# Performance work log

Hardware: AMD Instinct MI355X
Metric: run time of the kernel (lower is better)

Reference implementation:

```python
import jax, jax.numpy as jnp
import numpy as np

B, S, H, D = 2, 4096, 16, 128  # batch, seq, heads, head_dim
HID = H * D                    # 2048 hidden size
C = 128                        # chunk size for the chunked recurrent scan
EPS = 1e-6


def setup_inputs() -> dict:
    key = jax.random.key(0)
    ks = jax.random.split(key, 9)
    sc = 0.02  # initializer_range
    w = lambda k: jax.random.normal(k, (HID, HID), jnp.float32) * sc
    return {
        "x": jax.random.normal(ks[0], (B, S, HID), jnp.float32),
        "Wq": w(ks[1]), "bq": jnp.zeros((HID,), jnp.float32),
        "Wk": w(ks[2]), "bk": jnp.zeros((HID,), jnp.float32),
        "Wv": w(ks[3]), "bv": jnp.zeros((HID,), jnp.float32),
        "Wo": w(ks[4]), "bo": jnp.zeros((HID,), jnp.float32),
    }


def reference(x, Wq, bq, Wk, bk, Wv, bv, Wo, bo):
    Bx, Sx, hid = x.shape
    NC = Sx // C  # number of chunks

    q = (x @ Wq + bq).reshape(Bx, Sx, H, D)
    k = (x @ Wk + bk).reshape(Bx, Sx, H, D)
    v = (x @ Wv + bv).reshape(Bx, Sx, H, D)

    # positive feature map for linear attention
    qf = jax.nn.elu(q) + 1.0
    kf = jax.nn.elu(k) + 1.0

    # chunk: [B, NC, C, H, D]
    qf = qf.reshape(Bx, NC, C, H, D)
    kf = kf.reshape(Bx, NC, C, H, D)
    vc = v.reshape(Bx, NC, C, H, D)

    # inter-chunk recurrent state: exclusive cumulative sums of per-chunk KV outer
    kv = jnp.einsum('bnchd,bnche->bnhde', kf, vc)      # per-chunk KV state
    kv_ex = jnp.cumsum(kv, axis=1) - kv                # exclusive prefix state
    ksum = kf.sum(axis=2)                              # [B,NC,H,D]
    ksum_ex = jnp.cumsum(ksum, axis=1) - ksum          # exclusive normalizer state

    inter = jnp.einsum('bnchd,bnhde->bnche', qf, kv_ex)
    z_inter = jnp.einsum('bnchd,bnhd->bnch', qf, ksum_ex)

    # intra-chunk causal attention (masked matmul)
    A = jnp.einsum('bnchd,bnkhd->bnhck', qf, kf)       # [B,NC,H,C,C]
    causal = jnp.tril(jnp.ones((C, C), dtype=bool))
    A = jnp.where(causal[None, None, None], A, 0.0)
    intra = jnp.einsum('bnhck,bnkhe->bnche', A, vc)
    z_intra = jnp.swapaxes(A.sum(-1), 2, 3)            # [B,NC,C,H]

    out = (inter + intra) / (z_inter + z_intra + EPS)[..., None]
    out = out.reshape(Bx, Sx, hid)
    return out @ Wo + bo
```

## Files before the change

kernel.cpp:

```cpp
#include <hip/hip_runtime.h>

typedef unsigned short u16;
typedef unsigned int u32;
typedef unsigned long long u64;
typedef __attribute__((ext_vector_type(8))) short short8;
typedef __attribute__((ext_vector_type(4))) float f32x4;
typedef __attribute__((ext_vector_type(4))) int int4v;

constexpr int Bsz = 2, Ssz = 4096, Hn = 16, Dh = 128, HID = 2048;
constexpr int Cch = 128, NCh = 32;
constexpr float EPSf = 1e-6f;

#define MFMA16 __builtin_amdgcn_mfma_f32_16x16x32_bf16
#define VMCNT0 asm volatile("s_waitcnt vmcnt(0)" ::: "memory")

__device__ __forceinline__ float b2f(u16 u) {
  unsigned int i = ((unsigned int)u) << 16;
  return __builtin_bit_cast(float, i);
}
__device__ __forceinline__ u16 f2b(float f) {
  unsigned int i = __builtin_bit_cast(unsigned int, f);
  i += 0x7fffu + ((i >> 16) & 1u);
  return (u16)(i >> 16);
}

__device__ __forceinline__ void gload_lds16(const u16* g, u16* l) {
  __builtin_amdgcn_global_load_lds(
      (const __attribute__((address_space(1))) u32*)g,
      (__attribute__((address_space(3))) u32*)l, 16, 0, 0);
}

__global__ __launch_bounds__(256) void cvt_bf16(const float* __restrict__ x,
                                                u16* __restrict__ xb)
{
  const size_t n8 = (size_t)Bsz * Ssz * HID / 8;
  for (size_t i = (size_t)blockIdx.x * 256 + threadIdx.x; i < n8;
       i += (size_t)gridDim.x * 256) {
    const f32x4 a = *(const f32x4*)&x[i * 8];
    const f32x4 b = *(const f32x4*)&x[i * 8 + 4];
    u16 tmp[8];
#pragma unroll
    for (int u = 0; u < 4; ++u) { tmp[u] = f2b(a[u]); tmp[u + 4] = f2b(b[u]); }
    *(int4v*)&xb[i * 8] = *(const int4v*)tmp;
  }
}

__global__ __launch_bounds__(256) void transpose4(
    const float* __restrict__ A0, const float* __restrict__ A1,
    const float* __restrict__ A2, const float* __restrict__ A3,
    u16* __restrict__ T0, u16* __restrict__ T1,
    u16* __restrict__ T2, u16* __restrict__ T3)
{
  constexpr int N = HID, LDT = 72;
  const int z = blockIdx.z;
  const float* __restrict__ A = (z == 0) ? A0 : (z == 1) ? A1 : (z == 2) ? A2 : A3;
  u16* __restrict__ T = (z == 0) ? T0 : (z == 1) ? T1 : (z == 2) ? T2 : T3;
  __shared__ u16 lds[64 * LDT];
  const int t = threadIdx.x;
  const int i = t >> 3, j = (t & 7) * 8;
  const int r0 = blockIdx.y * 64, c0 = blockIdx.x * 64;
#pragma unroll
  for (int half = 0; half < 2; ++half) {
    const int r = i + half * 32;
    const f32x4 a = *(const f32x4*)&A[(size_t)(r0 + r) * N + c0 + j];
    const f32x4 b = *(const f32x4*)&A[(size_t)(r0 + r) * N + c0 + j + 4];
    u16 tmp[8];
#pragma unroll
    for (int u = 0; u < 4; ++u) { tmp[u] = f2b(a[u]); tmp[u + 4] = f2b(b[u]); }
    *(int4v*)&lds[r * LDT + j] = *(const int4v*)tmp;
  }
  __syncthreads();
#pragma unroll
  for (int half = 0; half < 2; ++half) {
    const int c = i + half * 32;
    u16 tmp[8];
#pragma unroll
    for (int u = 0; u < 8; ++u) tmp[u] = lds[(j + u) * LDT + c];
    *(int4v*)&T[(size_t)(c0 + c) * N + r0 + j] = *(const int4v*)tmp;
  }
}

template <int OUTF32>
__global__ __launch_bounds__(512) void gemm1b(
    const u16* __restrict__ A,
    const u16* __restrict__ W0T, const u16* __restrict__ W1T, const u16* __restrict__ W2T,
    const float* __restrict__ bb0, const float* __restrict__ bb1, const float* __restrict__ bb2,
    void* __restrict__ o0, void* __restrict__ o1, void* __restrict__ o2,
    int elu_mask)
{
  constexpr int K = HID, N = HID;
  constexpr int NT = K / 64;
  extern __shared__ u16 lds[];

  const int z = blockIdx.z;
  const u16* __restrict__ WT    = (z == 0) ? W0T : (z == 1) ? W1T : W2T;
  const float* __restrict__ bias = (z == 0) ? bb0 : (z == 1) ? bb1 : bb2;
  void* __restrict__ outv = (z == 0) ? o0 : (z == 1) ? o1 : o2;
  const bool elu = (elu_mask >> z) & 1;

  const int lid = blockIdx.x + 8 * blockIdx.y;
  const int wlid = (lid & 7) * 32 + (lid >> 3);
  const int n0 = (wlid >> 5) * 256;
  const int m0 = (wlid & 31) * 256;

  const int t = threadIdx.x, lane = t & 63, w = t >> 6;
  const int wm = w >> 2, wn = w & 3;
  const int l15 = lane & 15, lg = lane >> 4;
  const int sl2 = (l15 >> 1) & 3;

  const int strow = lane >> 2;
  const int stslot = (lane & 3) ^ ((lane >> 3) & 3);
  const u16* gA = A  + (size_t)(m0 + w * 16 + strow) * K + stslot * 8;
  const u16* gB = WT + (size_t)(n0 + w * 16 + strow) * K + stslot * 8;

  const int aRow = (wm * 128 + l15) * 32 + ((lg ^ sl2) << 3);
  const int bRow = 16384 + (wn * 64 + l15) * 32 + ((lg ^ sl2) << 3);
  u16* const lw = &lds[w * 512];

  f32x4 acc[8][4] = {};
  short8 aF[8], bF[4];

#define STAGE(SB, KKC) do {                                                   \
    gload_lds16(gA + (KKC) * 32,                 lw + (SB)*32768 + (KKC)*8192);          \
    gload_lds16(gA + (KKC) * 32 + (size_t)128*K, lw + (SB)*32768 + (KKC)*8192 + 4096);   \
    gload_lds16(gB + (KKC) * 32,                 lw + (SB)*32768 + 16384 + (KKC)*8192);  \
    gload_lds16(gB + (KKC) * 32 + (size_t)128*K, lw + (SB)*32768 + 16384 + (KKC)*8192 + 4096); \
  } while (0)

#define HALFBODY(BUF, KKC) do {                                               \
    _Pragma("unroll")                                                         \
    for (int i = 0; i < 8; ++i)                                               \
      aF[i] = *(const short8*)&lds[(BUF)*32768 + (KKC)*8192 + aRow + i*512];  \
    _Pragma("unroll")                                                         \
    for (int j = 0; j < 4; ++j)                                               \
      bF[j] = *(const short8*)&lds[(BUF)*32768 + (KKC)*8192 + bRow + j*512];  \
    __builtin_amdgcn_s_setprio(1);                                            \
    _Pragma("unroll")                                                         \
    for (int i = 0; i < 8; ++i) {                                             \
      acc[i][0] = MFMA16(aF[i], bF[0], acc[i][0], 0, 0, 0);                   \
      acc[i][1] = MFMA16(aF[i], bF[1], acc[i][1], 0, 0, 0);                   \
      acc[i][2] = MFMA16(aF[i], bF[2], acc[i][2], 0, 0, 0);                   \
      acc[i][3] = MFMA16(aF[i], bF[3], acc[i][3], 0, 0, 0);                   \
    }                                                                         \
    __builtin_amdgcn_s_setprio(0);                                            \
  } while (0)

#define WINDOW(BUF, PF) do {                                                  \
    VMCNT0;                                                                   \
    __builtin_amdgcn_s_barrier();                                             \
    if (PF) { STAGE((BUF)^1, 0); STAGE((BUF)^1, 1); gA += 64; gB += 64; }     \
    HALFBODY(BUF, 0);                                                         \
    HALFBODY(BUF, 1);                                                         \
  } while (0)

  STAGE(0, 0);
  STAGE(0, 1);
  gA += 64; gB += 64;

  for (int W = 0; W < NT; W += 2) {
    WINDOW(0, (W + 1) < NT);
    WINDOW(1, (W + 2) < NT);
  }

#pragma unroll
  for (int j = 0; j < 4; ++j) {
    const int col = n0 + wn * 64 + j * 16 + l15;
    const float bv = bias[col];
#pragma unroll
    for (int i = 0; i < 8; ++i) {
      const int row0 = m0 + wm * 128 + i * 16 + lg * 4;
#pragma unroll
      for (int r = 0; r < 4; ++r) {
        float v = acc[i][j][r] + bv;
        if (elu) v = (v > 0.0f) ? (v + 1.0f) : __expf(v);
        if (OUTF32) ((float*)outv)[(size_t)(row0 + r) * N + col] = v;
        else        ((u16*)outv)[(size_t)(row0 + r) * N + col] = f2b(v);
      }
    }
  }
#undef STAGE
#undef HALFBODY
#undef WINDOW
}

__global__ __launch_bounds__(256) void pass1_kv(
    const u16* __restrict__ KF, const u16* __restrict__ V,
    u16* __restrict__ KVT, float* __restrict__ KSUM)
{
  constexpr int LD = 136;
  __shared__ u16 lk[128 * LD];
  __shared__ u16 lv[128 * LD];
  __shared__ float kp[256];
  const int bnh = blockIdx.x;
  const int h = bnh % Hn, n = (bnh / Hn) % NCh, b = bnh / (Hn * NCh);
  const size_t rowbase = (size_t)(b * Ssz + n * Cch) * HID + h * Dh;
  const int t = threadIdx.x, lane = t & 63, w = t >> 6;
  const int wr = (w >> 1) * 64, wc = (w & 1) * 64;
  const int l15 = lane & 15, lg = lane >> 4;
  const int sr = t >> 4, sc = (t & 15) * 8;

#pragma unroll
  for (int rep = 0; rep < 8; ++rep) {
    const int r = rep * 16 + sr;
    *(int4v*)&lk[r * LD + sc] = *(const int4v*)&KF[rowbase + (size_t)r * HID + sc];
    *(int4v*)&lv[r * LD + sc] = *(const int4v*)&V[rowbase + (size_t)r * HID + sc];
  }
  __syncthreads();

  {
    const int col = t & 127, hf = t >> 7;
    float s = 0.0f;
    for (int c = hf * 64; c < hf * 64 + 64; ++c) s += b2f(lk[c * LD + col]);
    kp[t] = s;
  }
  __syncthreads();
  if (t < 128) KSUM[(size_t)bnh * Dh + t] = kp[t] + kp[t + 128];

  f32x4 acc[4][4] = {};
#pragma unroll
  for (int kk = 0; kk < 4; ++kk) {
    const int cb = kk * 32 + lg * 8;
    short8 aF[4], bF[4];
#pragma unroll
    for (int i = 0; i < 4; ++i) {
      const int e = wr + i * 16 + l15;
      short8 a;
#pragma unroll
      for (int u = 0; u < 8; ++u) a[u] = (short)lv[(cb + u) * LD + e];
      aF[i] = a;
    }
#pragma unroll
    for (int j = 0; j < 4; ++j) {
      const int d = wc + j * 16 + l15;
      short8 bb;
#pragma unroll
      for (int u = 0; u < 8; ++u) bb[u] = (short)lk[(cb + u) * LD + d];
      bF[j] = bb;
    }
#pragma unroll
    for (int i = 0; i < 4; ++i)
#pragma unroll
      for (int j = 0; j < 4; ++j)
        acc[i][j] = MFMA16(aF[i], bF[j], acc[i][j], 0, 0, 0);
  }

  u16* __restrict__ outp = KVT + (size_t)bnh * (Dh * Dh);
#pragma unroll
  for (int i = 0; i < 4; ++i) {
    const int e0 = wr + i * 16 + lg * 4;
#pragma unroll
    for (int j = 0; j < 4; ++j) {
      const int d = wc + j * 16 + l15;
#pragma unroll
      for (int r = 0; r < 4; ++r)
        outp[(size_t)(e0 + r) * Dh + d] = f2b(acc[i][j][r]);
    }
  }
}

__global__ __launch_bounds__(256) void cumsum_all(u16* __restrict__ KVT,
                                                  float* __restrict__ KS)
{
  const int nkv = (Bsz * Hn * Dh * Dh) / 256;
  if ((int)blockIdx.x < nkv) {
    const int tid = blockIdx.x * 256 + threadIdx.x;
    const int ed = tid & (Dh * Dh - 1);
    const int bh = tid >> 14;
    const int h = bh % Hn, b = bh / Hn;
    const size_t base = ((size_t)(b * NCh * Hn) + h) * (Dh * Dh) + ed;
    const size_t stride = (size_t)Hn * Dh * Dh;
    float s = 0.0f;
    for (int n = 0; n < NCh; ++n) {
      const size_t idx = base + (size_t)n * stride;
      const float v = b2f(KVT[idx]);
      KVT[idx] = f2b(s);
      s += v;
    }
  } else {
    const int tid = (blockIdx.x - nkv) * 256 + threadIdx.x;
    const int d = tid & (Dh - 1);
    const int bh = tid >> 7;
    const int h = bh % Hn, b = bh / Hn;
    const size_t base = ((size_t)(b * NCh * Hn) + h) * Dh + d;
    const size_t stride = (size_t)Hn * Dh;
    float s = 0.0f;
    for (int n = 0; n < NCh; ++n) {
      const size_t idx = base + (size_t)n * stride;
      const float v = KS[idx];
      KS[idx] = s;
      s += v;
    }
  }
}

__global__ __launch_bounds__(256) void pass2_attn(
    const u16* __restrict__ QF, const u16* __restrict__ KF, const u16* __restrict__ V,
    const u16* __restrict__ KVT, const float* __restrict__ KSE,
    u16* __restrict__ Y)
{
  constexpr int LD = 136;
  __shared__ u16 smem[4 * 128 * LD];
  __shared__ float zpart[2][128];
  u16* sQ  = smem;
  u16* sK  = smem + 128 * LD;
  u16* sA  = smem + 2 * 128 * LD;
  u16* sKV = smem + 3 * 128 * LD;

  const int bnh = blockIdx.x;
  const int h = bnh % Hn, n = (bnh / Hn) % NCh, b = bnh / (Hn * NCh);
  const size_t rowbase = (size_t)(b * Ssz + n * Cch) * HID + h * Dh;
  const int t = threadIdx.x, lane = t & 63, w = t >> 6;
  const int wr = (w >> 1) * 64, wc = (w & 1) * 64;
  const int l15 = lane & 15, lg = lane >> 4;
  const int sr = t >> 4, sc = (t & 15) * 8;

  const u16* __restrict__ kvsrc = KVT + (size_t)bnh * (Dh * Dh);
#pragma unroll
  for (int rep = 0; rep < 8; ++rep) {
    const int r = rep * 16 + sr;
    *(int4v*)&sQ[r * LD + sc]  = *(const int4v*)&QF[rowbase + (size_t)r * HID + sc];
    *(int4v*)&sK[r * LD + sc]  = *(const int4v*)&KF[rowbase + (size_t)r * HID + sc];
    *(int4v*)&sKV[r * LD + sc] = *(const int4v*)&kvsrc[r * Dh + sc];
  }
  __syncthreads();

  f32x4 acc[4][4] = {};
#pragma unroll
  for (int kk = 0; kk < 4; ++kk) {
    const int krd = kk * 32 + lg * 8;
    short8 aF[4], bF[4];
#pragma unroll
    for (int i = 0; i < 4; ++i)
      aF[i] = *(const short8*)&sQ[(wr + i * 16 + l15) * LD + krd];
#pragma unroll
    for (int j = 0; j < 4; ++j)
      bF[j] = *(const short8*)&sK[(wc + j * 16 + l15) * LD + krd];
#pragma unroll
    for (int i = 0; i < 4; ++i)
#pragma unroll
      for (int j = 0; j < 4; ++j)
        acc[i][j] = MFMA16(aF[i], bF[j], acc[i][j], 0, 0, 0);
  }
#pragma unroll
  for (int i = 0; i < 4; ++i) {
    const int c0 = wr + i * 16 + lg * 4;
#pragma unroll
    for (int j = 0; j < 4; ++j) {
      const int ck = wc + j * 16 + l15;
#pragma unroll
      for (int r = 0; r < 4; ++r) {
        const int c = c0 + r;
        sA[c * LD + ck] = f2b((ck <= c) ? acc[i][j][r] : 0.0f);
      }
    }
  }
  __syncthreads();

  if (t < 128) {
    const float* kse = KSE + (size_t)bnh * Dh;
    float zz = 0.0f;
    for (int d2 = 0; d2 < 128; ++d2) zz += b2f(sQ[t * LD + d2]) * kse[d2];
    zpart[0][t] = zz;
  } else {
    const int row = t - 128;
    float zz = 0.0f;
    for (int ck = 0; ck < 128; ++ck) zz += b2f(sA[row * LD + ck]);
    zpart[1][row] = zz;
  }
#pragma unroll
  for (int rep = 0; rep < 8; ++rep) {
    const int r = rep * 16 + sr;
    *(int4v*)&sK[r * LD + sc] = *(const int4v*)&V[rowbase + (size_t)r * HID + sc];
  }
  __syncthreads();

  f32x4 o[4][4] = {};
#pragma unroll
  for (int kk = 0; kk < 4; ++kk) {
    const int krd = kk * 32 + lg * 8;
    short8 aF[4], bF[4];
#pragma unroll
    for (int i = 0; i < 4; ++i)
      aF[i] = *(const short8*)&sA[(wr + i * 16 + l15) * LD + krd];
#pragma unroll
    for (int j = 0; j < 4; ++j) {
      const int e = wc + j * 16 + l15;
      short8 bb;
#pragma unroll
      for (int u = 0; u < 8; ++u) bb[u] = (short)sK[(krd + u) * LD + e];
      bF[j] = bb;
    }
#pragma unroll
    for (int i = 0; i < 4; ++i)
#pragma unroll
      for (int j = 0; j < 4; ++j)
        o[i][j] = MFMA16(aF[i], bF[j], o[i][j], 0, 0, 0);
  }
#pragma unroll
  for (int kk = 0; kk < 4; ++kk) {
    const int krd = kk * 32 + lg * 8;
    short8 aF[4], bF[4];
#pragma unroll
    for (int i = 0; i < 4; ++i)
      aF[i] = *(const short8*)&sQ[(wr + i * 16 + l15) * LD + krd];
#pragma unroll
    for (int j = 0; j < 4; ++j)
      bF[j] = *(const short8*)&sKV[(wc + j * 16 + l15) * LD + krd];
#pragma unroll
    for (int i = 0; i < 4; ++i)
#pragma unroll
      for (int j = 0; j < 4; ++j)
        o[i][j] = MFMA16(aF[i], bF[j], o[i][j], 0, 0, 0);
  }

#pragma unroll
  for (int i = 0; i < 4; ++i) {
    const int c0 = wr + i * 16 + lg * 4;
#pragma unroll
    for (int j = 0; j < 4; ++j) {
      const int e = wc + j * 16 + l15;
#pragma unroll
      for (int r = 0; r < 4; ++r) {
        const int c = c0 + r;
        const float zz = zpart[0][c] + zpart[1][c] + EPSf;
        Y[rowbase + (size_t)c * HID + e] = f2b(o[i][j][r] / zz);
      }
    }
  }
}

extern "C" void kernel_launch(void* const* d_in, const int* in_sizes, int n_in,
                              void* d_out, int out_size, void* d_ws, size_t ws_size,
                              hipStream_t stream)
{
  const float* x  = (const float*)d_in[0];
  const float* Wq = (const float*)d_in[1];
  const float* bq = (const float*)d_in[2];
  const float* Wk = (const float*)d_in[3];
  const float* bk = (const float*)d_in[4];
  const float* Wv = (const float*)d_in[5];
  const float* bv = (const float*)d_in[6];
  const float* Wo = (const float*)d_in[7];
  const float* bo = (const float*)d_in[8];
  float* out = (float*)d_out;

  char* p = (char*)d_ws;
  auto take = [&](size_t bytes) { char* q = p; p += (bytes + 255) & ~(size_t)255; return q; };
  u16* WqT = (u16*)take((size_t)HID * HID * 2);
  u16* WkT = (u16*)take((size_t)HID * HID * 2);
  u16* WvT = (u16*)take((size_t)HID * HID * 2);
  u16* WoT = (u16*)take((size_t)HID * HID * 2);
  u16* QF  = (u16*)take((size_t)Bsz * Ssz * HID * 2);
  u16* KFb = (u16*)take((size_t)Bsz * Ssz * HID * 2);
  u16* Vb  = (u16*)take((size_t)Bsz * Ssz * HID * 2);
  char* region = take((size_t)Bsz * Ssz * HID * 2);
  u16* xb  = (u16*)region;
  u16* KVT = (u16*)region;
  float* KS = (float*)take((size_t)Bsz * NCh * Hn * Dh * 4);
  u16* Yb = QF;

  (void)hipFuncSetAttribute((const void*)gemm1b<0>,
                            hipFuncAttributeMaxDynamicSharedMemorySize, 131072);
  (void)hipFuncSetAttribute((const void*)gemm1b<1>,
                            hipFuncAttributeMaxDynamicSharedMemorySize, 131072);

  dim3 blk(256, 1, 1);
  cvt_bf16<<<dim3(2048), blk, 0, stream>>>(x, xb);
  transpose4<<<dim3(HID / 64, HID / 64, 4), blk, 0, stream>>>(
      Wq, Wk, Wv, Wo, WqT, WkT, WvT, WoT);
  gemm1b<0><<<dim3(HID / 256, (Bsz * Ssz) / 256, 3), dim3(512), 131072, stream>>>(
      xb, WqT, WkT, WvT, bq, bk, bv, QF, KFb, Vb, 0x3);
  pass1_kv<<<dim3(Bsz * NCh * Hn), blk, 0, stream>>>(KFb, Vb, KVT, KS);
  cumsum_all<<<dim3((Bsz * Hn * Dh * Dh) / 256 + (Bsz * Hn * Dh) / 256), blk, 0, stream>>>(KVT, KS);
  pass2_attn<<<dim3(Bsz * NCh * Hn), blk, 0, stream>>>(QF, KFb, Vb, KVT, KS, Yb);
  gemm1b<1><<<dim3(HID / 256, (Bsz * Ssz) / 256, 1), dim3(512), 131072, stream>>>(
      Yb, WoT, WoT, WoT, bo, bo, bo, out, out, out, 0);
}
```

Before: 421.0 us.

## Deepen GEMM pipeline to four LDS stages with partial vmcnt waits

The projection GEMM now prefetches over a four-buffer ring of 32-wide K slices instead of double-buffering 64-wide slices. It waits with partial vmcnt counts, so up to three stages of global-to-LDS loads stay in flight while the MFMAs run, rather than draining every load at each window. Barriers now come once per 32-wide K slice instead of once per 64-wide window. The block-to-tile mapping is also changed to regroup tiles for L2 locality.

After: 400.2 us. 4.9% less time.

```diff
diff --git a/kernel.cpp b/kernel.cpp
--- a/kernel.cpp
+++ b/kernel.cpp
@@ -12,7 +12,7 @@
 constexpr float EPSf = 1e-6f;
 
 #define MFMA16 __builtin_amdgcn_mfma_f32_16x16x32_bf16
-#define VMCNT0 asm volatile("s_waitcnt vmcnt(0)" ::: "memory")
+#define VMW(N) asm volatile("s_waitcnt vmcnt(" #N ")" ::: "memory")
 
 __device__ __forceinline__ float b2f(u16 u) {
   unsigned int i = ((unsigned int)u) << 16;
@@ -81,7 +81,7 @@
 }
 
 template <int OUTF32>
-__global__ __launch_bounds__(512) void gemm1b(
+__global__ __launch_bounds__(512) void gemm4b(
     const u16* __restrict__ A,
     const u16* __restrict__ W0T, const u16* __restrict__ W1T, const u16* __restrict__ W2T,
     const float* __restrict__ bb0, const float* __restrict__ bb1, const float* __restrict__ bb2,
@@ -89,7 +89,6 @@
     int elu_mask)
 {
   constexpr int K = HID, N = HID;
-  constexpr int NT = K / 64;
   extern __shared__ u16 lds[];
 
   const int z = blockIdx.z;
@@ -99,9 +98,9 @@
   const bool elu = (elu_mask >> z) & 1;
 
   const int lid = blockIdx.x + 8 * blockIdx.y;
-  const int wlid = (lid & 7) * 32 + (lid >> 3);
-  const int n0 = (wlid >> 5) * 256;
-  const int m0 = (wlid & 31) * 256;
+  const int k8 = lid & 7, j32 = lid >> 3;
+  const int m0 = (k8 * 4 + (j32 >> 3)) * 256;
+  const int n0 = (j32 & 7) * 256;
 
   const int t = threadIdx.x, lane = t & 63, w = t >> 6;
   const int wm = w >> 2, wn = w & 3;
@@ -114,26 +113,30 @@
   const u16* gB = WT + (size_t)(n0 + w * 16 + strow) * K + stslot * 8;
 
   const int aRow = (wm * 128 + l15) * 32 + ((lg ^ sl2) << 3);
-  const int bRow = 16384 + (wn * 64 + l15) * 32 + ((lg ^ sl2) << 3);
+  const int bRow = 8192 + (wn * 64 + l15) * 32 + ((lg ^ sl2) << 3);
   u16* const lw = &lds[w * 512];
 
   f32x4 acc[8][4] = {};
   short8 aF[8], bF[4];
 
-#define STAGE(SB, KKC) do {                                                   \
-    gload_lds16(gA + (KKC) * 32,                 lw + (SB)*32768 + (KKC)*8192);          \
-    gload_lds16(gA + (KKC) * 32 + (size_t)128*K, lw + (SB)*32768 + (KKC)*8192 + 4096);   \
-    gload_lds16(gB + (KKC) * 32,                 lw + (SB)*32768 + 16384 + (KKC)*8192);  \
-    gload_lds16(gB + (KKC) * 32 + (size_t)128*K, lw + (SB)*32768 + 16384 + (KKC)*8192 + 4096); \
+#define STAGE4(SB) do {                                                       \
+    gload_lds16(gA,                   lw + (SB)*16384);                       \
+    gload_lds16(gA + (size_t)128*K,   lw + (SB)*16384 + 4096);                \
+    gload_lds16(gB,                   lw + (SB)*16384 + 8192);                \
+    gload_lds16(gB + (size_t)128*K,   lw + (SB)*16384 + 8192 + 4096);         \
+    gA += 32; gB += 32;                                                       \
   } while (0)
 
-#define HALFBODY(BUF, KKC) do {                                               \
+#define WINDOW(BUF, SB, PF, VMN) do {                                         \
+    VMW(VMN);                                                                 \
+    __builtin_amdgcn_s_barrier();                                             \
+    if (PF) STAGE4(SB);                                                       \
     _Pragma("unroll")                                                         \
     for (int i = 0; i < 8; ++i)                                               \
-      aF[i] = *(const short8*)&lds[(BUF)*32768 + (KKC)*8192 + aRow + i*512];  \
+      aF[i] = *(const short8*)&lds[(BUF)*16384 + aRow + i*512];               \
     _Pragma("unroll")                                                         \
     for (int j = 0; j < 4; ++j)                                               \
-      bF[j] = *(const short8*)&lds[(BUF)*32768 + (KKC)*8192 + bRow + j*512];  \
+      bF[j] = *(const short8*)&lds[(BUF)*16384 + bRow + j*512];               \
     __builtin_amdgcn_s_setprio(1);                                            \
     _Pragma("unroll")                                                         \
     for (int i = 0; i < 8; ++i) {                                             \
@@ -145,22 +148,20 @@
     __builtin_amdgcn_s_setprio(0);                                            \
   } while (0)
 
-#define WINDOW(BUF, PF) do {                                                  \
-    VMCNT0;                                                                   \
-    __builtin_amdgcn_s_barrier();                                             \
-    if (PF) { STAGE((BUF)^1, 0); STAGE((BUF)^1, 1); gA += 64; gB += 64; }     \
-    HALFBODY(BUF, 0);                                                         \
-    HALFBODY(BUF, 1);                                                         \
-  } while (0)
-
-  STAGE(0, 0);
-  STAGE(0, 1);
-  gA += 64; gB += 64;
-
-  for (int W = 0; W < NT; W += 2) {
-    WINDOW(0, (W + 1) < NT);
-    WINDOW(1, (W + 2) < NT);
-  }
+  STAGE4(0);
+  STAGE4(1);
+  STAGE4(2);
+
+  for (int W = 0; W < 60; W += 4) {
+    WINDOW(0, 3, 1, 8);
+    WINDOW(1, 0, 1, 8);
+    WINDOW(2, 1, 1, 8);
+    WINDOW(3, 2, 1, 8);
+  }
+  WINDOW(0, 3, 1, 8);
+  WINDOW(1, 0, 0, 8);
+  WINDOW(2, 0, 0, 4);
+  WINDOW(3, 0, 0, 0);
 
 #pragma unroll
   for (int j = 0; j < 4; ++j) {
@@ -178,8 +179,7 @@
       }
     }
   }
-#undef STAGE
-#undef HALFBODY
+#undef STAGE4
 #undef WINDOW
 }
 
@@ -459,20 +459,20 @@
   float* KS = (float*)take((size_t)Bsz * NCh * Hn * Dh * 4);
   u16* Yb = QF;
 
-  (void)hipFuncSetAttribute((const void*)gemm1b<0>,
+  (void)hipFuncSetAttribute((const void*)gemm4b<0>,
                             hipFuncAttributeMaxDynamicSharedMemorySize, 131072);
-  (void)hipFuncSetAttribute((const void*)gemm1b<1>,
+  (void)hipFuncSetAttribute((const void*)gemm4b<1>,
                             hipFuncAttributeMaxDynamicSharedMemorySize, 131072);
 
   dim3 blk(256, 1, 1);
   cvt_bf16<<<dim3(2048), blk, 0, stream>>>(x, xb);
   transpose4<<<dim3(HID / 64, HID / 64, 4), blk, 0, stream>>>(
       Wq, Wk, Wv, Wo, WqT, WkT, WvT, WoT);
-  gemm1b<0><<<dim3(HID / 256, (Bsz * Ssz) / 256, 3), dim3(512), 131072, stream>>>(
+  gemm4b<0><<<dim3(HID / 256, (Bsz * Ssz) / 256, 3), dim3(512), 131072, stream>>>(
       xb, WqT, WkT, WvT, bq, bk, bv, QF, KFb, Vb, 0x3);
   pass1_kv<<<dim3(Bsz * NCh * Hn), blk, 0, stream>>>(KFb, Vb, KVT, KS);
   cumsum_all<<<dim3((Bsz * Hn * Dh * Dh) / 256 + (Bsz * Hn * Dh) / 256), blk, 0, stream>>>(KVT, KS);
   pass2_attn<<<dim3(Bsz * NCh * Hn), blk, 0, stream>>>(QF, KFb, Vb, KVT, KS, Yb);
-  gemm1b<1><<<dim3(HID / 256, (Bsz * Ssz) / 256, 1), dim3(512), 131072, stream>>>(
+  gemm4b<1><<<dim3(HID / 256, (Bsz * Ssz) / 256, 1), dim3(512), 131072, stream>>>(
       Yb, WoT, WoT, WoT, bo, bo, bo, out, out, out, 0);
 }
```
